# Kernel optimization log

Hardware: AMD Instinct MI355X
Metric: run time of the kernel (lower is better)

The kernel has to match this reference:

```python
import jax, jax.numpy as jnp
import numpy as np

N = 20000      # atom nodes
E_UND = 200000 # undirected edges -> E = 2*E_UND directed, stored as interleaved reverse pairs
D = 128        # hid_dim
H = 4          # heads (fixed in MVMP)
DEPTH = 3


def _build_graph():
    rng = np.random.default_rng(0)
    u_chain = np.arange(N - 1)
    v_chain = u_chain + 1
    n_extra = E_UND - (N - 1)
    ue = rng.integers(0, N, n_extra)
    ve = rng.integers(0, N, n_extra)
    ve = np.where(ue == ve, (ve + 1) % N, ve)
    u = np.concatenate([u_chain, ue])
    v = np.concatenate([v_chain, ve])
    # interleave so that edge 2k = u->v and edge 2k+1 = v->u (reverse_edge pairing)
    src = np.stack([u, v], 1).reshape(-1).astype(np.int32)
    dst = np.stack([v, u], 1).reshape(-1).astype(np.int32)
    return jnp.asarray(src), jnp.asarray(dst)


def setup_inputs() -> dict:
    key = jax.random.key(0)
    ks = jax.random.split(key, 10)
    src, dst = _build_graph()
    E = src.shape[0]
    s = 1.0 / np.sqrt(D)

    def lin(k, shape):
        return (jax.random.normal(k, shape, jnp.float32) * s).astype(jnp.float32)

    return {
        "f": jax.random.normal(ks[0], (N, D), jnp.float32),
        "x": jax.random.normal(ks[1], (E, D), jnp.float32),
        "src": src,
        "dst": dst,
        "Wq": lin(ks[2], (D, D)), "bq": jnp.zeros((D,), jnp.float32),
        "Wk": lin(ks[3], (D, D)), "bk": jnp.zeros((D,), jnp.float32),
        "Wv": lin(ks[4], (D, D)), "bv": jnp.zeros((D,), jnp.float32),
        "Wo": lin(ks[5], (D, D)), "bo": jnp.zeros((D,), jnp.float32),
        "W_mp": lin(ks[6], (DEPTH - 1, D, D)),
        "b_mp": jnp.zeros((DEPTH - 1, D), jnp.float32),
        "W_last": lin(ks[7], (3 * D, D)),
        "b_last": jnp.zeros((D,), jnp.float32),
    }


def _mailbox_attention(f_h, h, dst, Wq, bq, Wk, bk, Wv, bv, Wo, bo):
    """add_attn: per-node MHA with query = node state, keys/values = incoming edge msgs.
    Implemented as an edge-segment softmax (no padding), equivalent to DGL degree bucketing."""
    n = f_h.shape[0]
    dk = D // H
    q = (f_h @ Wq + bq).reshape(n, H, dk)     # [N,H,dk]
    k = (h @ Wk + bk).reshape(-1, H, dk)      # [E,H,dk]
    v = (h @ Wv + bv).reshape(-1, H, dk)      # [E,H,dk]
    scores = jnp.einsum("ehd,ehd->eh", q[dst], k) / jnp.sqrt(jnp.float32(dk))  # [E,H]
    smax = jax.ops.segment_max(scores, dst, num_segments=n)   # [N,H]
    p = jnp.exp(scores - smax[dst])
    denom = jax.ops.segment_sum(p, dst, num_segments=n)       # [N,H]
    ctx = jax.ops.segment_sum(p[:, :, None] * v, dst, num_segments=n) / denom[:, :, None]
    out = ctx.reshape(n, D) @ Wo + bo
    return out + f_h  # residual in add_attn


def reference(f, x, src, dst, Wq, bq, Wk, bk, Wv, bv, Wo, bo, W_mp, b_mp, W_last, b_last):
    n, E = f.shape[0], x.shape[0]
    f_h = f          # init_node: f_h = f.clone()
    h = x            # init_edge: h = x.clone()
    for i in range(DEPTH - 1):
        # multi_update_all: copy_e('h','m') then add_attn on node states
        f_h = _mailbox_attention(f_h, h, dst, Wq, bq, Wk, bk, Wv, bv, Wo, bo)
        # rev_h = reverse_edge(h): swap interleaved pairs
        rev_h = h.reshape(E // 2, 2, D)[:, ::-1, :].reshape(E, D)
        # del_reverse_message: m = f_h[src] - rev_h
        m = f_h[src] - rev_h
        # update_edge: h = relu(x + Linear_i(m))
        h = jax.nn.relu(x + m @ W_mp[i] + b_mp[i])
    # final: copy_e('h','mail') then update_node with Linear(3D->D)
    mail = jax.ops.segment_sum(h, dst, num_segments=n)
    return jnp.concatenate([mail, f_h, f], axis=1) @ W_last + b_last
```

## Files before the change

### kernel.cpp

```cpp
#include <hip/hip_runtime.h>
#include <hip/hip_bf16.h>

typedef __attribute__((ext_vector_type(8))) short bf16x8;
typedef __attribute__((ext_vector_type(4))) float f32x4;

__device__ __forceinline__ unsigned short f2bf(float f) {
    unsigned u = __float_as_uint(f);
    unsigned r = (u + 0x7FFFu + ((u >> 16) & 1u)) >> 16;
    return (unsigned short)r;
}
__device__ __forceinline__ float bf2f(unsigned short b) {
    return __uint_as_float(((unsigned)b) << 16);
}
__device__ __forceinline__ unsigned pack2(float a, float b) {
    return (unsigned)f2bf(a) | ((unsigned)f2bf(b) << 16);
}
__device__ __forceinline__ unsigned pksub(unsigned a, unsigned b) {
    float r0 = bf2f((unsigned short)(a & 0xffff)) - bf2f((unsigned short)(b & 0xffff));
    float r1 = bf2f((unsigned short)(a >> 16))    - bf2f((unsigned short)(b >> 16));
    return pack2(r0, r1);
}
#define EXP2(x) __builtin_amdgcn_exp2f(x)

__device__ __forceinline__ void gload_lds16(const void* g, void* l) {
    __builtin_amdgcn_global_load_lds(
        (const __attribute__((address_space(1))) unsigned int*)g,
        (__attribute__((address_space(3))) unsigned int*)l,
        16, 0, 0);
}

__global__ __launch_bounds__(512, 2) void gemm_q512(
    const unsigned short* __restrict__ A, const unsigned short* __restrict__ WT,
    const float* __restrict__ bias, unsigned short* __restrict__ out, int M)
{
    __shared__ __align__(16) unsigned short As[64 * 128];

    const int t = threadIdx.x, wave = t >> 6, lane = t & 63;
    const int lr = lane & 15, lk = lane >> 4;

    bf16x8 Bf[4][4];
    f32x4 bs[4];
#pragma unroll
    for (int fn = 0; fn < 4; fn++) {
        const int col0 = wave * 64 + fn * 16 + lk * 4;
        bs[fn] = *reinterpret_cast<const f32x4*>(bias + col0);
        const int n = wave * 64 + fn * 16 + lr;
#pragma unroll
        for (int kk = 0; kk < 4; kk++)
            Bf[kk][fn] = *reinterpret_cast<const bf16x8*>(WT + n * 128 + kk * 32 + lk * 8);
    }

    const int row0 = blockIdx.x * 64;
#pragma unroll
    for (int i = 0; i < 2; i++) {
        const int flat = (i * 512 + t) * 16;
        const int r = flat >> 8, c = (flat >> 4) & 15;
        int gr = row0 + r; if (gr >= M) gr = M - 1;
        const void* g = A + (size_t)gr * 128 + ((c ^ (r & 7)) << 3);
        void* l = (void*)((char*)&As[0] + (size_t)(i * 512 + wave * 64) * 16 + 0);
        gload_lds16(g, l);
    }
    __syncthreads();

    f32x4 acc[4][4];
#pragma unroll
    for (int a = 0; a < 4; a++)
#pragma unroll
        for (int b = 0; b < 4; b++) acc[a][b] = (f32x4){0.f, 0.f, 0.f, 0.f};

#pragma unroll
    for (int kk = 0; kk < 4; kk++) {
        bf16x8 af[4];
#pragma unroll
        for (int fm = 0; fm < 4; fm++) {
            const int r = fm * 16 + lr;
            const int c = (kk * 4 + lk) ^ (r & 7);
            af[fm] = *reinterpret_cast<const bf16x8*>(&As[r * 128 + c * 8]);
        }
#pragma unroll
        for (int fm = 0; fm < 4; fm++)
#pragma unroll
            for (int fn = 0; fn < 4; fn++)
                acc[fm][fn] = __builtin_amdgcn_mfma_f32_16x16x32_bf16(
                    Bf[kk][fn], af[fm], acc[fm][fn], 0, 0, 0);
    }

#pragma unroll
    for (int fm = 0; fm < 4; fm++) {
        const int row = row0 + fm * 16 + lr;
        if (row < M) {
#pragma unroll
            for (int fn = 0; fn < 4; fn++) {
                const int col0 = wave * 64 + fn * 16 + lk * 4;
                f32x4 vv = acc[fm][fn] + bs[fn];
                uint2 o; o.x = pack2(vv[0], vv[1]); o.y = pack2(vv[2], vv[3]);
                *reinterpret_cast<uint2*>(out + (size_t)row * 512 + col0) = o;
            }
        }
    }
}

__global__ __launch_bounds__(256, 2) void gemm_k512(
    const unsigned short* __restrict__ A, const unsigned short* __restrict__ WT,
    const float* __restrict__ bias, float* __restrict__ f_h,
    unsigned short* __restrict__ f_hb, int M)
{
    __shared__ __align__(16) unsigned short As[64 * 512];

    const int t = threadIdx.x, wave = t >> 6, lane = t & 63;
    const int lr = lane & 15, lk = lane >> 4;

    bf16x8 Bf[16][2];
    f32x4 bs[2];
#pragma unroll
    for (int fn = 0; fn < 2; fn++) {
        const int col0 = wave * 32 + fn * 16 + lk * 4;
        bs[fn] = *reinterpret_cast<const f32x4*>(bias + col0);
        const int n = wave * 32 + fn * 16 + lr;
#pragma unroll
        for (int kk = 0; kk < 16; kk++)
            Bf[kk][fn] = *reinterpret_cast<const bf16x8*>(WT + n * 512 + kk * 32 + lk * 8);
    }

    const int row0 = blockIdx.x * 64;
#pragma unroll
    for (int i = 0; i < 16; i++) {
        const int flat = (i * 256 + t) * 16;
        const int r = flat >> 10, c = (flat >> 4) & 63;
        int gr = row0 + r; if (gr >= M) gr = M - 1;
        const void* g = A + (size_t)gr * 512 + ((c ^ (r & 7)) << 3);
        void* l = (void*)((char*)&As[0] + (size_t)(i * 256 + wave * 64) * 16);
        gload_lds16(g, l);
    }
    __syncthreads();

    f32x4 acc[4][2];
#pragma unroll
    for (int a = 0; a < 4; a++)
#pragma unroll
        for (int b = 0; b < 2; b++) acc[a][b] = (f32x4){0.f, 0.f, 0.f, 0.f};

#pragma unroll
    for (int kk = 0; kk < 16; kk++) {
        bf16x8 af[4];
#pragma unroll
        for (int fm = 0; fm < 4; fm++) {
            const int r = fm * 16 + lr;
            const int c = (kk * 4 + lk) ^ (r & 7);
            af[fm] = *reinterpret_cast<const bf16x8*>(&As[r * 512 + c * 8]);
        }
#pragma unroll
        for (int fm = 0; fm < 4; fm++)
#pragma unroll
            for (int fn = 0; fn < 2; fn++)
                acc[fm][fn] = __builtin_amdgcn_mfma_f32_16x16x32_bf16(
                    Bf[kk][fn], af[fm], acc[fm][fn], 0, 0, 0);
    }

#pragma unroll
    for (int fm = 0; fm < 4; fm++) {
        const int row = row0 + fm * 16 + lr;
        if (row < M) {
#pragma unroll
            for (int fn = 0; fn < 2; fn++) {
                const int col0 = wave * 32 + fn * 16 + lk * 4;
                const size_t off = (size_t)row * 128 + col0;
                f32x4 vv = acc[fm][fn] + bs[fn];
                vv += *reinterpret_cast<const f32x4*>(f_h + off);
                *reinterpret_cast<f32x4*>(f_h + off) = vv;
                uint2 o; o.x = pack2(vv[0], vv[1]); o.y = pack2(vv[2], vv[3]);
                *reinterpret_cast<uint2*>(f_hb + off) = o;
            }
        }
    }
}

__global__ __launch_bounds__(256, 3) void gemm_mrelu(
    const unsigned short* __restrict__ f_hb, const unsigned short* __restrict__ h,
    const int* __restrict__ src, const unsigned short* __restrict__ WT,
    const float* __restrict__ bias, const unsigned short* __restrict__ resx,
    unsigned short* __restrict__ out, int E, int ntiles)
{
    __shared__ __align__(16) unsigned short As[2][64 * 128];

    const int t = threadIdx.x, wave = t >> 6, lane = t & 63;
    const int lr = lane & 15, lk = lane >> 4;

    bf16x8 Bf[4][2];
    f32x4 bs[2];
#pragma unroll
    for (int fn = 0; fn < 2; fn++) {
        const int col0 = wave * 32 + fn * 16 + lk * 4;
        bs[fn] = *reinterpret_cast<const f32x4*>(bias + col0);
        const int n = wave * 32 + fn * 16 + lr;
#pragma unroll
        for (int kk = 0; kk < 4; kk++)
            Bf[kk][fn] = *reinterpret_cast<const bf16x8*>(WT + n * 128 + kk * 32 + lk * 8);
    }

    uint4 Lh[4], Lf[4];
    auto load_t = [&](int row0) {
#pragma unroll
        for (int i = 0; i < 4; i++) {
            const int flat = (wave * 4 + i) * 1024 + lane * 16;
            const int r = flat >> 8, c = (flat >> 4) & 15;
            int e = row0 + r; if (e >= E) e = E - 1;
            Lh[i] = *reinterpret_cast<const uint4*>(h + (size_t)(e ^ 1) * 128 + c * 8);
            const int se = src[e];
            Lf[i] = *reinterpret_cast<const uint4*>(f_hb + (size_t)se * 128 + c * 8);
        }
    };
    auto write_t = [&](int buf) {
#pragma unroll
        for (int i = 0; i < 4; i++) {
            const int flat = (wave * 4 + i) * 1024 + lane * 16;
            const int r = flat >> 8, c = (flat >> 4) & 15;
            uint4 d;
            d.x = pksub(Lf[i].x, Lh[i].x); d.y = pksub(Lf[i].y, Lh[i].y);
            d.z = pksub(Lf[i].z, Lh[i].z); d.w = pksub(Lf[i].w, Lh[i].w);
            *reinterpret_cast<uint4*>(&As[buf][r * 128 + ((c ^ (r & 7)) << 3)]) = d;
        }
    };

    int tt = blockIdx.x;
    if (tt >= ntiles) return;
    load_t(tt * 64);
    write_t(0);
    int cur = 0;
    __syncthreads();

    for (; tt < ntiles; tt += gridDim.x) {
        const int nxt = tt + gridDim.x;
        if (nxt < ntiles) load_t(nxt * 64);

        f32x4 acc[4][2];
#pragma unroll
        for (int a = 0; a < 4; a++)
#pragma unroll
            for (int b = 0; b < 2; b++) acc[a][b] = (f32x4){0.f, 0.f, 0.f, 0.f};

#pragma unroll
        for (int kk = 0; kk < 4; kk++) {
            bf16x8 af[4];
#pragma unroll
            for (int fm = 0; fm < 4; fm++) {
                const int r = fm * 16 + lr;
                const int c = (kk * 4 + lk) ^ (r & 7);
                af[fm] = *reinterpret_cast<const bf16x8*>(&As[cur][r * 128 + c * 8]);
            }
#pragma unroll
            for (int fm = 0; fm < 4; fm++)
#pragma unroll
                for (int fn = 0; fn < 2; fn++)
                    acc[fm][fn] = __builtin_amdgcn_mfma_f32_16x16x32_bf16(
                        Bf[kk][fn], af[fm], acc[fm][fn], 0, 0, 0);
        }

        const int row0 = tt * 64;
#pragma unroll
        for (int fm = 0; fm < 4; fm++) {
            const int row = row0 + fm * 16 + lr;
            if (row < E) {
#pragma unroll
                for (int fn = 0; fn < 2; fn++) {
                    const int col0 = wave * 32 + fn * 16 + lk * 4;
                    const size_t off = (size_t)row * 128 + col0;
                    f32x4 vv = acc[fm][fn] + bs[fn];
                    uint2 rb = *reinterpret_cast<const uint2*>(resx + off);
                    vv[0] += bf2f((unsigned short)(rb.x & 0xffff));
                    vv[1] += bf2f((unsigned short)(rb.x >> 16));
                    vv[2] += bf2f((unsigned short)(rb.y & 0xffff));
                    vv[3] += bf2f((unsigned short)(rb.y >> 16));
                    vv[0] = fmaxf(vv[0], 0.f); vv[1] = fmaxf(vv[1], 0.f);
                    vv[2] = fmaxf(vv[2], 0.f); vv[3] = fmaxf(vv[3], 0.f);
                    uint2 o; o.x = pack2(vv[0], vv[1]); o.y = pack2(vv[2], vv[3]);
                    *reinterpret_cast<uint2*>(out + off) = o;
                }
            }
        }

        if (nxt < ntiles) write_t(cur ^ 1);
        __syncthreads();
        cur ^= 1;
    }
}

__global__ __launch_bounds__(256, 2) void gemm_final(
    const unsigned short* __restrict__ A0, const unsigned short* __restrict__ A1,
    const unsigned short* __restrict__ A2,
    const unsigned short* __restrict__ W0T, const unsigned short* __restrict__ W1T,
    const unsigned short* __restrict__ W2T,
    const float* __restrict__ bias, float* __restrict__ out, int M)
{
    __shared__ __align__(16) unsigned short As[3][64 * 128];

    const int t = threadIdx.x, wave = t >> 6, lane = t & 63;
    const int lr = lane & 15, lk = lane >> 4;

    const unsigned short* Asrc[3] = { A0, A1, A2 };
    const unsigned short* Wsrc[3] = { W0T, W1T, W2T };

    bf16x8 Bf[12][2];
    f32x4 bs[2];
#pragma unroll
    for (int fn = 0; fn < 2; fn++) {
        const int col0 = wave * 32 + fn * 16 + lk * 4;
        bs[fn] = *reinterpret_cast<const f32x4*>(bias + col0);
        const int n = wave * 32 + fn * 16 + lr;
#pragma unroll
        for (int b = 0; b < 3; b++)
#pragma unroll
            for (int kk = 0; kk < 4; kk++)
                Bf[b * 4 + kk][fn] = *reinterpret_cast<const bf16x8*>(
                    Wsrc[b] + n * 128 + kk * 32 + lk * 8);
    }

    const int row0 = blockIdx.x * 64;
#pragma unroll
    for (int b = 0; b < 3; b++) {
#pragma unroll
        for (int i = 0; i < 4; i++) {
            const int flat = (wave * 4 + i) * 1024 + lane * 16;
            const int r = flat >> 8, c = (flat >> 4) & 15;
            int gr = row0 + r; if (gr >= M) gr = M - 1;
            const void* g = Asrc[b] + (size_t)gr * 128 + ((c ^ (r & 7)) << 3);
            void* l = (void*)((char*)&As[b][0] + (size_t)(wave * 4 + i) * 1024);
            gload_lds16(g, l);
        }
    }
    __syncthreads();

    f32x4 acc[4][2];
#pragma unroll
    for (int a = 0; a < 4; a++)
#pragma unroll
        for (int b = 0; b < 2; b++) acc[a][b] = (f32x4){0.f, 0.f, 0.f, 0.f};

#pragma unroll
    for (int b = 0; b < 3; b++) {
#pragma unroll
        for (int kk = 0; kk < 4; kk++) {
            bf16x8 af[4];
#pragma unroll
            for (int fm = 0; fm < 4; fm++) {
                const int r = fm * 16 + lr;
                const int c = (kk * 4 + lk) ^ (r & 7);
                af[fm] = *reinterpret_cast<const bf16x8*>(&As[b][r * 128 + c * 8]);
            }
#pragma unroll
            for (int fm = 0; fm < 4; fm++)
#pragma unroll
                for (int fn = 0; fn < 2; fn++)
                    acc[fm][fn] = __builtin_amdgcn_mfma_f32_16x16x32_bf16(
                        Bf[b * 4 + kk][fn], af[fm], acc[fm][fn], 0, 0, 0);
        }
    }

#pragma unroll
    for (int fm = 0; fm < 4; fm++) {
        const int row = row0 + fm * 16 + lr;
        if (row < M) {
#pragma unroll
            for (int fn = 0; fn < 2; fn++) {
                const int col0 = wave * 32 + fn * 16 + lk * 4;
                *reinterpret_cast<f32x4*>(out + (size_t)row * 128 + col0) =
                    acc[fm][fn] + bs[fn];
            }
        }
    }
}

__global__ void hist_kernel(const int* __restrict__ dst, int* __restrict__ deg, int E_) {
    int e = blockIdx.x * 256 + threadIdx.x;
    if (e < E_) atomicAdd(&deg[dst[e]], 1);
}

__global__ __launch_bounds__(1024) void scan_kernel(
    const int* __restrict__ deg, int* __restrict__ rowptr,
    int* __restrict__ cursor, int N_)
{
    __shared__ int part[1024];
    const int t = threadIdx.x;
    const int chunk = (N_ + 1023) >> 10;
    const int base = t * chunk;
    int s = 0;
    for (int i = 0; i < chunk; i++) {
        int idx = base + i;
        if (idx < N_) s += deg[idx];
    }
    part[t] = s;
    __syncthreads();
    for (int off = 1; off < 1024; off <<= 1) {
        int v = (t >= off) ? part[t - off] : 0;
        __syncthreads();
        part[t] += v;
        __syncthreads();
    }
    int run = (t == 0) ? 0 : part[t - 1];
    for (int i = 0; i < chunk; i++) {
        int idx = base + i;
        if (idx < N_) {
            rowptr[idx] = run;
            cursor[idx] = run;
            run += deg[idx];
        }
    }
    if (t == 1023) rowptr[N_] = part[1023];
}

__global__ void scatter_kernel(const int* __restrict__ dst, int* __restrict__ cursor,
                               int* __restrict__ eidx, int E_) {
    int e = blockIdx.x * 256 + threadIdx.x;
    if (e >= E_) return;
    int pos = atomicAdd(&cursor[dst[e]], 1);
    eidx[pos] = e;
}

__global__ __launch_bounds__(256) void attn_fused(
    const unsigned short* __restrict__ qkt, const unsigned short* __restrict__ h,
    const int* __restrict__ rowptr, const int* __restrict__ eidx,
    unsigned short* __restrict__ whm, int N_)
{
    const int n = blockIdx.x * 4 + (threadIdx.x >> 6);
    if (n >= N_) return;
    const int lane = threadIdx.x & 63;
    const int g = lane >> 4, s = lane & 15;

    const int beg = rowptr[n], end = rowptr[n + 1];
    unsigned short* outp = whm + (size_t)n * 512 + g * 128 + s * 8;
    if (beg == end) {
        *reinterpret_cast<uint2*>(outp) = make_uint2(0u, 0u);
        *reinterpret_cast<uint2*>(outp + 4) = make_uint2(0u, 0u);
        return;
    }

    float qk[4][8];
#pragma unroll
    for (int hd = 0; hd < 4; hd++) {
        uint4 u = *reinterpret_cast<const uint4*>(qkt + (size_t)n * 512 + hd * 128 + s * 8);
        qk[hd][0] = bf2f((unsigned short)(u.x & 0xffff)); qk[hd][1] = bf2f((unsigned short)(u.x >> 16));
        qk[hd][2] = bf2f((unsigned short)(u.y & 0xffff)); qk[hd][3] = bf2f((unsigned short)(u.y >> 16));
        qk[hd][4] = bf2f((unsigned short)(u.z & 0xffff)); qk[hd][5] = bf2f((unsigned short)(u.z >> 16));
        qk[hd][6] = bf2f((unsigned short)(u.w & 0xffff)); qk[hd][7] = bf2f((unsigned short)(u.w >> 16));
    }

    float m[4], l[4], a[4][8];
#pragma unroll
    for (int hd = 0; hd < 4; hd++) {
        m[hd] = -3.0e38f; l[hd] = 0.f;
#pragma unroll
        for (int j = 0; j < 8; j++) a[hd][j] = 0.f;
    }

    const int T = (end - beg + 3) >> 2;
    int idx = beg + g;
    uint4 hv = make_uint4(0u, 0u, 0u, 0u);
    if (idx < end) hv = *reinterpret_cast<const uint4*>(h + (size_t)eidx[idx] * 128 + s * 8);

    for (int it = 0; it < T; it++) {
        const uint4 hc = hv;
        const bool valid = (idx < end);
        const int nidx = idx + 4;
        if (nidx < end) hv = *reinterpret_cast<const uint4*>(h + (size_t)eidx[nidx] * 128 + s * 8);
        idx = nidx;

        float hf[8];
        hf[0] = bf2f((unsigned short)(hc.x & 0xffff)); hf[1] = bf2f((unsigned short)(hc.x >> 16));
        hf[2] = bf2f((unsigned short)(hc.y & 0xffff)); hf[3] = bf2f((unsigned short)(hc.y >> 16));
        hf[4] = bf2f((unsigned short)(hc.z & 0xffff)); hf[5] = bf2f((unsigned short)(hc.z >> 16));
        hf[6] = bf2f((unsigned short)(hc.w & 0xffff)); hf[7] = bf2f((unsigned short)(hc.w >> 16));

        float part[4];
#pragma unroll
        for (int hd = 0; hd < 4; hd++) {
            float pp = 0.f;
#pragma unroll
            for (int j = 0; j < 8; j++) pp += qk[hd][j] * hf[j];
            part[hd] = pp;
        }
#pragma unroll
        for (int off = 1; off < 16; off <<= 1) {
#pragma unroll
            for (int hd = 0; hd < 4; hd++)
                part[hd] += __shfl_xor(part[hd], off, 64);
        }

        if (valid) {
#pragma unroll
            for (int hd = 0; hd < 4; hd++) {
                const float sv = part[hd];
                const float mn = fmaxf(m[hd], sv);
                const float sc = EXP2(m[hd] - mn);
                const float pp = EXP2(sv - mn);
                l[hd] = l[hd] * sc + pp;
#pragma unroll
                for (int j = 0; j < 8; j++) a[hd][j] = a[hd][j] * sc + pp * hf[j];
                m[hd] = mn;
            }
        }
    }

#pragma unroll
    for (int off = 16; off <= 32; off <<= 1) {
#pragma unroll
        for (int hd = 0; hd < 4; hd++) {
            const float mo = __shfl_xor(m[hd], off, 64);
            const float lo = __shfl_xor(l[hd], off, 64);
            const float mn = fmaxf(m[hd], mo);
            const float sc = EXP2(m[hd] - mn);
            const float so = EXP2(mo - mn);
            l[hd] = l[hd] * sc + lo * so;
#pragma unroll
            for (int j = 0; j < 8; j++) {
                const float ao = __shfl_xor(a[hd][j], off, 64);
                a[hd][j] = a[hd][j] * sc + ao * so;
            }
            m[hd] = mn;
        }
    }

#pragma unroll
    for (int hd = 0; hd < 4; hd++) {
        if (g == hd) {
            const float rl = 1.f / l[hd];
            uint4 o;
            o.x = pack2(a[hd][0] * rl, a[hd][1] * rl);
            o.y = pack2(a[hd][2] * rl, a[hd][3] * rl);
            o.z = pack2(a[hd][4] * rl, a[hd][5] * rl);
            o.w = pack2(a[hd][6] * rl, a[hd][7] * rl);
            *reinterpret_cast<uint4*>(outp) = o;
        }
    }
}

__global__ __launch_bounds__(256) void mail_csr(
    const unsigned short* __restrict__ h,
    const int* __restrict__ rowptr, const int* __restrict__ eidx,
    unsigned short* __restrict__ mailb, int N_)
{
    const int n = blockIdx.x * 4 + (threadIdx.x >> 6);
    if (n >= N_) return;
    const int lane = threadIdx.x & 63;
    const int g = lane >> 4, s = lane & 15;

    const int beg = rowptr[n], end = rowptr[n + 1];

    float a[8];
#pragma unroll
    for (int j = 0; j < 8; j++) a[j] = 0.f;

    const int T = (end - beg + 3) >> 2;
    int idx = beg + g;
    uint4 hv = make_uint4(0u, 0u, 0u, 0u);
    if (idx < end) hv = *reinterpret_cast<const uint4*>(h + (size_t)eidx[idx] * 128 + s * 8);

    for (int it = 0; it < T; it++) {
        const uint4 hc = hv;
        const bool valid = (idx < end);
        const int nidx = idx + 4;
        if (nidx < end) hv = *reinterpret_cast<const uint4*>(h + (size_t)eidx[nidx] * 128 + s * 8);
        idx = nidx;
        if (valid) {
            a[0] += bf2f((unsigned short)(hc.x & 0xffff)); a[1] += bf2f((unsigned short)(hc.x >> 16));
            a[2] += bf2f((unsigned short)(hc.y & 0xffff)); a[3] += bf2f((unsigned short)(hc.y >> 16));
            a[4] += bf2f((unsigned short)(hc.z & 0xffff)); a[5] += bf2f((unsigned short)(hc.z >> 16));
            a[6] += bf2f((unsigned short)(hc.w & 0xffff)); a[7] += bf2f((unsigned short)(hc.w >> 16));
        }
    }
#pragma unroll
    for (int off = 16; off <= 32; off <<= 1)
#pragma unroll
        for (int j = 0; j < 8; j++) a[j] += __shfl_xor(a[j], off, 64);

    if (g == 0) {
        uint4 o;
        o.x = pack2(a[0], a[1]); o.y = pack2(a[2], a[3]);
        o.z = pack2(a[4], a[5]); o.w = pack2(a[6], a[7]);
        *reinterpret_cast<uint4*>(mailb + (size_t)n * 128 + s * 8) = o;
    }
}

struct W5 { const float* p[5]; };

__global__ void cvt_wT(W5 w, unsigned short* __restrict__ out) {
    const float* src = w.p[blockIdx.x];
    unsigned short* dst = out + (size_t)blockIdx.x * 16384;
    for (int idx = threadIdx.x; idx < 16384; idx += 256) {
        const int k = idx >> 7, n = idx & 127;
        dst[n * 128 + k] = f2bf(src[idx]);
    }
}

#define SCORE_SCALE 0.25508994161f

__global__ void mcat_kernel(const float* __restrict__ Wq, const float* __restrict__ Wk,
                            const float* __restrict__ bq,
                            unsigned short* __restrict__ McatT, float* __restrict__ cbias) {
    const int oc = blockIdx.x;
    const int hd = oc >> 7, ip = oc & 127;
    const int a = threadIdx.x;
    const float* wk = Wk + ip * 128 + hd * 32;
    const float* wq = Wq + a * 128 + hd * 32;
    float s = 0.f;
    for (int jj = 0; jj < 32; jj++) s += wq[jj] * wk[jj];
    McatT[(size_t)oc * 128 + a] = f2bf(s * SCORE_SCALE);
    if (a == 0) {
        float c = 0.f;
        for (int jj = 0; jj < 32; jj++) c += bq[hd * 32 + jj] * wk[jj];
        cbias[oc] = c * SCORE_SCALE;
    }
}

__global__ void pcat_kernel(const float* __restrict__ Wv, const float* __restrict__ Wo,
                            unsigned short* __restrict__ PcatT) {
    const int j = blockIdx.x;
    const int k = threadIdx.x;
    const int hd = k >> 7, i = k & 127;
    float s = 0.f;
    for (int cc = 0; cc < 32; cc++)
        s += Wv[i * 128 + hd * 32 + cc] * Wo[(hd * 32 + cc) * 128 + j];
    PcatT[(size_t)j * 512 + k] = f2bf(s);
}

__global__ void bias2_kernel(const float* __restrict__ bv, const float* __restrict__ Wo,
                             const float* __restrict__ bo, float* __restrict__ bias2) {
    const int j = threadIdx.x;
    if (j >= 128) return;
    float s = 0.f;
    for (int c = 0; c < 128; c++) s += bv[c] * Wo[c * 128 + j];
    bias2[j] = s + bo[j];
}

__global__ void cvt_bf16(const float* __restrict__ in, unsigned short* __restrict__ out, long n4) {
    long i = (long)blockIdx.x * 256 + threadIdx.x;
    if (i >= n4) return;
    float4 v = reinterpret_cast<const float4*>(in)[i];
    ushort4 o;
    o.x = f2bf(v.x); o.y = f2bf(v.y); o.z = f2bf(v.z); o.w = f2bf(v.w);
    reinterpret_cast<ushort4*>(out)[i] = o;
}

__global__ void prep_f(const float* __restrict__ f, unsigned short* __restrict__ fb,
                       float* __restrict__ f_h, int n4) {
    int i = blockIdx.x * 256 + threadIdx.x;
    if (i >= n4) return;
    float4 v = reinterpret_cast<const float4*>(f)[i];
    reinterpret_cast<float4*>(f_h)[i] = v;
    ushort4 o;
    o.x = f2bf(v.x); o.y = f2bf(v.y); o.z = f2bf(v.z); o.w = f2bf(v.w);
    reinterpret_cast<ushort4*>(fb)[i] = o;
}

extern "C" void kernel_launch(void* const* d_in, const int* in_sizes, int n_in,
                              void* d_out, int out_size, void* d_ws, size_t ws_size,
                              hipStream_t stream)
{
    const float* f      = (const float*)d_in[0];
    const float* x      = (const float*)d_in[1];
    const int*   src    = (const int*)d_in[2];
    const int*   dst    = (const int*)d_in[3];
    const float* Wq     = (const float*)d_in[4];
    const float* bq     = (const float*)d_in[5];
    const float* Wk     = (const float*)d_in[6];
    const float* bk     = (const float*)d_in[7];
    const float* Wv     = (const float*)d_in[8];
    const float* bv     = (const float*)d_in[9];
    const float* Wo     = (const float*)d_in[10];
    const float* bo     = (const float*)d_in[11];
    const float* W_mp   = (const float*)d_in[12];
    const float* b_mp   = (const float*)d_in[13];
    const float* W_last = (const float*)d_in[14];
    const float* b_last = (const float*)d_in[15];
    (void)bk;

    const int N = in_sizes[0] / 128;
    const int E = in_sizes[1] / 128;

    char* p = (char*)d_ws;
    auto take = [&](size_t bytes) { char* r = p; p += (bytes + 255) & ~(size_t)255; return r; };
    unsigned short* w5T   = (unsigned short*)take(5 * 16384 * 2);
    unsigned short* McatT = (unsigned short*)take(512 * 128 * 2);
    unsigned short* PcatT = (unsigned short*)take(128 * 512 * 2);
    float* cbias  = (float*)take(512 * 4);
    float* bias2  = (float*)take(128 * 4);
    unsigned short* xb    = (unsigned short*)take((size_t)E * 128 * 2);
    unsigned short* h1    = (unsigned short*)take((size_t)E * 128 * 2);
    unsigned short* h2    = (unsigned short*)take((size_t)E * 128 * 2);
    unsigned short* fb    = (unsigned short*)take((size_t)N * 128 * 2);
    unsigned short* f_hb  = (unsigned short*)take((size_t)N * 128 * 2);
    unsigned short* qkt   = (unsigned short*)take((size_t)N * 512 * 2);
    unsigned short* whm   = (unsigned short*)take((size_t)N * 512 * 2);
    unsigned short* mailb = (unsigned short*)take((size_t)N * 128 * 2);
    float* f_h    = (float*)take((size_t)N * 128 * 4);
    int* deg      = (int*)take((size_t)N * 4);
    int* rowptr   = (int*)take((size_t)(N + 1) * 4);
    int* cursor   = (int*)take((size_t)N * 4);
    int* eidx     = (int*)take((size_t)E * 4);

    const unsigned short* Wm0T = w5T + 0 * 16384;
    const unsigned short* Wm1T = w5T + 1 * 16384;
    const unsigned short* WL0T = w5T + 2 * 16384;
    const unsigned short* WL1T = w5T + 3 * 16384;
    const unsigned short* WL2T = w5T + 4 * 16384;

    W5 w5;
    w5.p[0] = W_mp; w5.p[1] = W_mp + 16384;
    w5.p[2] = W_last; w5.p[3] = W_last + 16384; w5.p[4] = W_last + 32768;

    cvt_wT<<<5, 256, 0, stream>>>(w5, w5T);
    mcat_kernel<<<512, 128, 0, stream>>>(Wq, Wk, bq, McatT, cbias);
    pcat_kernel<<<128, 512, 0, stream>>>(Wv, Wo, PcatT);
    bias2_kernel<<<1, 128, 0, stream>>>(bv, Wo, bo, bias2);
    cvt_bf16<<<(int)(((long)E * 32 + 255) / 256), 256, 0, stream>>>(x, xb, (long)E * 32);
    prep_f<<<(N * 32 + 255) / 256, 256, 0, stream>>>(f, fb, f_h, N * 32);

    hipMemsetAsync(deg, 0, (size_t)N * 4, stream);
    hist_kernel<<<(E + 255) / 256, 256, 0, stream>>>(dst, deg, E);
    scan_kernel<<<1, 1024, 0, stream>>>(deg, rowptr, cursor, N);
    scatter_kernel<<<(E + 255) / 256, 256, 0, stream>>>(dst, cursor, eidx, E);

    const int ntN = (N + 63) / 64;
    const int ntE = (E + 63) / 64;
    const int gNode = (N + 3) / 4;
    const int gMrelu = (ntE < 1280) ? ntE : 1280;

    const unsigned short* hc = xb;
    unsigned short* houts[2] = { h1, h2 };
    for (int it = 0; it < 2; it++) {
        const unsigned short* fh_in = (it == 0) ? fb : f_hb;
        gemm_q512<<<ntN, 512, 0, stream>>>(fh_in, McatT, cbias, qkt, N);
        attn_fused<<<gNode, 256, 0, stream>>>(qkt, hc, rowptr, eidx, whm, N);
        gemm_k512<<<ntN, 256, 0, stream>>>(whm, PcatT, bias2, f_h, f_hb, N);
        gemm_mrelu<<<gMrelu, 256, 0, stream>>>(
            f_hb, hc, src, (it == 0) ? Wm0T : Wm1T, b_mp + (size_t)it * 128,
            xb, houts[it], E, ntE);
        hc = houts[it];
    }

    mail_csr<<<gNode, 256, 0, stream>>>(hc, rowptr, eidx, mailb, N);

    gemm_final<<<ntN, 256, 0, stream>>>(
        mailb, f_hb, fb, WL0T, WL1T, WL2T, b_last, (float*)d_out, N);
}
```

Before: 554.9 us.

## Split edge GEMM by linearity: precompute f_h@W per node, gather result

Uses linearity, (f_h[src]-rev_h)@W = (f_h@W)[src] - rev_h@W. A new small node GEMM computes f_h@W once per node, and the edge GEMM then streams h straight into LDS with async global-to-LDS loads. The reverse-pair swap is handled by reading row lr^1 from LDS, and the per-node product is gathered in the epilogue. The attention cross-lane reduction is also restructured into a butterfly that exchanges fewer values, and the edge-kernel grid size changes. The cost is an extra kernel launch plus an extra rounding of the node product to bf16.

```diff
diff --git a/kernel.cpp b/kernel.cpp
--- a/kernel.cpp
+++ b/kernel.cpp
@@ -14,11 +14,6 @@
 }
 __device__ __forceinline__ unsigned pack2(float a, float b) {
     return (unsigned)f2bf(a) | ((unsigned)f2bf(b) << 16);
-}
-__device__ __forceinline__ unsigned pksub(unsigned a, unsigned b) {
-    float r0 = bf2f((unsigned short)(a & 0xffff)) - bf2f((unsigned short)(b & 0xffff));
-    float r1 = bf2f((unsigned short)(a >> 16))    - bf2f((unsigned short)(b >> 16));
-    return pack2(r0, r1);
 }
 #define EXP2(x) __builtin_amdgcn_exp2f(x)
 
@@ -27,6 +22,16 @@
         (const __attribute__((address_space(1))) unsigned int*)g,
         (__attribute__((address_space(3))) unsigned int*)l,
         16, 0, 0);
+}
+
+__device__ __forceinline__ void mergeSt(float& Km, float& Kl, float (&Ka)[8],
+                                        float rm, float rl, const float (&ra)[8]) {
+    const float mn = fmaxf(Km, rm);
+    const float c1 = EXP2(Km - mn), c2 = EXP2(rm - mn);
+    Kl = Kl * c1 + rl * c2;
+#pragma unroll
+    for (int j = 0; j < 8; j++) Ka[j] = Ka[j] * c1 + ra[j] * c2;
+    Km = mn;
 }
 
 __global__ __launch_bounds__(512, 2) void gemm_q512(
@@ -175,9 +180,78 @@
     }
 }
 
-__global__ __launch_bounds__(256, 3) void gemm_mrelu(
-    const unsigned short* __restrict__ f_hb, const unsigned short* __restrict__ h,
-    const int* __restrict__ src, const unsigned short* __restrict__ WT,
+__global__ __launch_bounds__(256, 2) void gemm_n128(
+    const unsigned short* __restrict__ A, const unsigned short* __restrict__ WT,
+    unsigned short* __restrict__ out, int M)
+{
+    __shared__ __align__(16) unsigned short As[64 * 128];
+
+    const int t = threadIdx.x, wave = t >> 6, lane = t & 63;
+    const int lr = lane & 15, lk = lane >> 4;
+
+    bf16x8 Bf[4][2];
+#pragma unroll
+    for (int fn = 0; fn < 2; fn++) {
+        const int n = wave * 32 + fn * 16 + lr;
+#pragma unroll
+        for (int kk = 0; kk < 4; kk++)
+            Bf[kk][fn] = *reinterpret_cast<const bf16x8*>(WT + n * 128 + kk * 32 + lk * 8);
+    }
+
+    const int row0 = blockIdx.x * 64;
+#pragma unroll
+    for (int i = 0; i < 4; i++) {
+        const int flat = (wave * 4 + i) * 1024 + lane * 16;
+        const int r = flat >> 8, c = (flat >> 4) & 15;
+        int gr = row0 + r; if (gr >= M) gr = M - 1;
+        const void* g = A + (size_t)gr * 128 + ((c ^ (r & 7)) << 3);
+        void* l = (void*)((char*)&As[0] + (size_t)(wave * 4 + i) * 1024);
+        gload_lds16(g, l);
+    }
+    __syncthreads();
+
+    f32x4 acc[4][2];
+#pragma unroll
+    for (int a = 0; a < 4; a++)
+#pragma unroll
+        for (int b = 0; b < 2; b++) acc[a][b] = (f32x4){0.f, 0.f, 0.f, 0.f};
+
+#pragma unroll
+    for (int kk = 0; kk < 4; kk++) {
+        bf16x8 af[4];
+#pragma unroll
+        for (int fm = 0; fm < 4; fm++) {
+            const int r = fm * 16 + lr;
+            const int c = (kk * 4 + lk) ^ (r & 7);
+            af[fm] = *reinterpret_cast<const bf16x8*>(&As[r * 128 + c * 8]);
+        }
+#pragma unroll
+        for (int fm = 0; fm < 4; fm++)
+#pragma unroll
+            for (int fn = 0; fn < 2; fn++)
+                acc[fm][fn] = __builtin_amdgcn_mfma_f32_16x16x32_bf16(
+                    Bf[kk][fn], af[fm], acc[fm][fn], 0, 0, 0);
+    }
+
+#pragma unroll
+    for (int fm = 0; fm < 4; fm++) {
+        const int row = row0 + fm * 16 + lr;
+        if (row < M) {
+#pragma unroll
+            for (int fn = 0; fn < 2; fn++) {
+                const int col0 = wave * 32 + fn * 16 + lk * 4;
+                uint2 o;
+                o.x = pack2(acc[fm][fn][0], acc[fm][fn][1]);
+                o.y = pack2(acc[fm][fn][2], acc[fm][fn][3]);
+                *reinterpret_cast<uint2*>(out + (size_t)row * 128 + col0) = o;
+            }
+        }
+    }
+}
+
+__global__ __launch_bounds__(256, 3) void gemm_hw(
+    const unsigned short* __restrict__ h, const int* __restrict__ src,
+    const unsigned short* __restrict__ gnb, const unsigned short* __restrict__ WT,
     const float* __restrict__ bias, const unsigned short* __restrict__ resx,
     unsigned short* __restrict__ out, int E, int ntiles)
 {
@@ -198,40 +272,40 @@
             Bf[kk][fn] = *reinterpret_cast<const bf16x8*>(WT + n * 128 + kk * 32 + lk * 8);
     }
 
-    uint4 Lh[4], Lf[4];
-    auto load_t = [&](int row0) {
+    auto stage = [&](int buf, int row0) {
 #pragma unroll
         for (int i = 0; i < 4; i++) {
             const int flat = (wave * 4 + i) * 1024 + lane * 16;
             const int r = flat >> 8, c = (flat >> 4) & 15;
-            int e = row0 + r; if (e >= E) e = E - 1;
-            Lh[i] = *reinterpret_cast<const uint4*>(h + (size_t)(e ^ 1) * 128 + c * 8);
-            const int se = src[e];
-            Lf[i] = *reinterpret_cast<const uint4*>(f_hb + (size_t)se * 128 + c * 8);
-        }
-    };
-    auto write_t = [&](int buf) {
-#pragma unroll
-        for (int i = 0; i < 4; i++) {
-            const int flat = (wave * 4 + i) * 1024 + lane * 16;
-            const int r = flat >> 8, c = (flat >> 4) & 15;
-            uint4 d;
-            d.x = pksub(Lf[i].x, Lh[i].x); d.y = pksub(Lf[i].y, Lh[i].y);
-            d.z = pksub(Lf[i].z, Lh[i].z); d.w = pksub(Lf[i].w, Lh[i].w);
-            *reinterpret_cast<uint4*>(&As[buf][r * 128 + ((c ^ (r & 7)) << 3)]) = d;
+            int gr = row0 + r; if (gr >= E) gr = E - 1;
+            const void* g = h + (size_t)gr * 128 + ((c ^ (r & 7)) << 3);
+            void* l = (void*)((char*)&As[buf][0] + (size_t)(wave * 4 + i) * 1024);
+            gload_lds16(g, l);
         }
     };
 
     int tt = blockIdx.x;
     if (tt >= ntiles) return;
-    load_t(tt * 64);
-    write_t(0);
+    stage(0, tt * 64);
+    __syncthreads();
     int cur = 0;
-    __syncthreads();
 
     for (; tt < ntiles; tt += gridDim.x) {
         const int nxt = tt + gridDim.x;
-        if (nxt < ntiles) load_t(nxt * 64);
+        if (nxt < ntiles) stage(cur ^ 1, nxt * 64);
+
+        const int row0 = tt * 64;
+
+        uint2 gnv[4][2];
+#pragma unroll
+        for (int fm = 0; fm < 4; fm++) {
+            int row = row0 + fm * 16 + lr; if (row >= E) row = E - 1;
+            const int sr = src[row];
+#pragma unroll
+            for (int fn = 0; fn < 2; fn++)
+                gnv[fm][fn] = *reinterpret_cast<const uint2*>(
+                    gnb + (size_t)sr * 128 + wave * 32 + fn * 16 + lk * 4);
+        }
 
         f32x4 acc[4][2];
 #pragma unroll
@@ -244,9 +318,9 @@
             bf16x8 af[4];
 #pragma unroll
             for (int fm = 0; fm < 4; fm++) {
-                const int r = fm * 16 + lr;
-                const int c = (kk * 4 + lk) ^ (r & 7);
-                af[fm] = *reinterpret_cast<const bf16x8*>(&As[cur][r * 128 + c * 8]);
+                const int rr = fm * 16 + (lr ^ 1);
+                const int cc = (kk * 4 + lk) ^ (rr & 7);
+                af[fm] = *reinterpret_cast<const bf16x8*>(&As[cur][rr * 128 + cc * 8]);
             }
 #pragma unroll
             for (int fm = 0; fm < 4; fm++)
@@ -256,7 +330,6 @@
                         Bf[kk][fn], af[fm], acc[fm][fn], 0, 0, 0);
         }
 
-        const int row0 = tt * 64;
 #pragma unroll
         for (int fm = 0; fm < 4; fm++) {
             const int row = row0 + fm * 16 + lr;
@@ -265,8 +338,13 @@
                 for (int fn = 0; fn < 2; fn++) {
                     const int col0 = wave * 32 + fn * 16 + lk * 4;
                     const size_t off = (size_t)row * 128 + col0;
-                    f32x4 vv = acc[fm][fn] + bs[fn];
-                    uint2 rb = *reinterpret_cast<const uint2*>(resx + off);
+                    f32x4 vv = bs[fn] - acc[fm][fn];
+                    const uint2 gb = gnv[fm][fn];
+                    vv[0] += bf2f((unsigned short)(gb.x & 0xffff));
+                    vv[1] += bf2f((unsigned short)(gb.x >> 16));
+                    vv[2] += bf2f((unsigned short)(gb.y & 0xffff));
+                    vv[3] += bf2f((unsigned short)(gb.y >> 16));
+                    const uint2 rb = *reinterpret_cast<const uint2*>(resx + off);
                     vv[0] += bf2f((unsigned short)(rb.x & 0xffff));
                     vv[1] += bf2f((unsigned short)(rb.x >> 16));
                     vv[2] += bf2f((unsigned short)(rb.y & 0xffff));
@@ -279,7 +357,6 @@
             }
         }
 
-        if (nxt < ntiles) write_t(cur ^ 1);
         __syncthreads();
         cur ^= 1;
     }
@@ -500,37 +577,53 @@
         }
     }
 
-#pragma unroll
-    for (int off = 16; off <= 32; off <<= 1) {
-#pragma unroll
-        for (int hd = 0; hd < 4; hd++) {
-            const float mo = __shfl_xor(m[hd], off, 64);
-            const float lo = __shfl_xor(l[hd], off, 64);
-            const float mn = fmaxf(m[hd], mo);
-            const float sc = EXP2(m[hd] - mn);
-            const float so = EXP2(mo - mn);
-            l[hd] = l[hd] * sc + lo * so;
-#pragma unroll
-            for (int j = 0; j < 8; j++) {
-                const float ao = __shfl_xor(a[hd][j], off, 64);
-                a[hd][j] = a[hd][j] * sc + ao * so;
-            }
-            m[hd] = mn;
-        }
-    }
-
-#pragma unroll
-    for (int hd = 0; hd < 4; hd++) {
-        if (g == hd) {
-            const float rl = 1.f / l[hd];
-            uint4 o;
-            o.x = pack2(a[hd][0] * rl, a[hd][1] * rl);
-            o.y = pack2(a[hd][2] * rl, a[hd][3] * rl);
-            o.z = pack2(a[hd][4] * rl, a[hd][5] * rl);
-            o.w = pack2(a[hd][6] * rl, a[hd][7] * rl);
-            *reinterpret_cast<uint4*>(outp) = o;
-        }
-    }
+    const bool lo = (g < 2);
+    const bool evn = ((g & 1) == 0);
+    float kAm = lo ? m[0] : m[2], kAl = lo ? l[0] : l[2];
+    float kBm = lo ? m[1] : m[3], kBl = lo ? l[1] : l[3];
+    float sAm = lo ? m[2] : m[0], sAl = lo ? l[2] : l[0];
+    float sBm = lo ? m[3] : m[1], sBl = lo ? l[3] : l[1];
+    float kAa[8], kBa[8], sAa[8], sBa[8];
+#pragma unroll
+    for (int j = 0; j < 8; j++) {
+        kAa[j] = lo ? a[0][j] : a[2][j];
+        kBa[j] = lo ? a[1][j] : a[3][j];
+        sAa[j] = lo ? a[2][j] : a[0][j];
+        sBa[j] = lo ? a[3][j] : a[1][j];
+    }
+    {
+        float rm = __shfl_xor(sAm, 32, 64), rl = __shfl_xor(sAl, 32, 64);
+        float ra[8];
+#pragma unroll
+        for (int j = 0; j < 8; j++) ra[j] = __shfl_xor(sAa[j], 32, 64);
+        mergeSt(kAm, kAl, kAa, rm, rl, ra);
+        rm = __shfl_xor(sBm, 32, 64); rl = __shfl_xor(sBl, 32, 64);
+#pragma unroll
+        for (int j = 0; j < 8; j++) ra[j] = __shfl_xor(sBa[j], 32, 64);
+        mergeSt(kBm, kBl, kBa, rm, rl, ra);
+    }
+    float Km = evn ? kAm : kBm, Kl = evn ? kAl : kBl;
+    float Sm = evn ? kBm : kAm, Sl = evn ? kBl : kAl;
+    float Ka[8], Sa[8];
+#pragma unroll
+    for (int j = 0; j < 8; j++) {
+        Ka[j] = evn ? kAa[j] : kBa[j];
+        Sa[j] = evn ? kBa[j] : kAa[j];
+    }
+    {
+        float rm = __shfl_xor(Sm, 16, 64), rl = __shfl_xor(Sl, 16, 64);
+        float ra[8];
+#pragma unroll
+        for (int j = 0; j < 8; j++) ra[j] = __shfl_xor(Sa[j], 16, 64);
+        mergeSt(Km, Kl, Ka, rm, rl, ra);
+    }
+    const float rl_ = 1.f / Kl;
+    uint4 o;
+    o.x = pack2(Ka[0] * rl_, Ka[1] * rl_);
+    o.y = pack2(Ka[2] * rl_, Ka[3] * rl_);
+    o.z = pack2(Ka[4] * rl_, Ka[5] * rl_);
+    o.w = pack2(Ka[6] * rl_, Ka[7] * rl_);
+    *reinterpret_cast<uint4*>(outp) = o;
 }
 
 __global__ __launch_bounds__(256) void mail_csr(
@@ -688,6 +781,7 @@
     unsigned short* h2    = (unsigned short*)take((size_t)E * 128 * 2);
     unsigned short* fb    = (unsigned short*)take((size_t)N * 128 * 2);
     unsigned short* f_hb  = (unsigned short*)take((size_t)N * 128 * 2);
+    unsigned short* gnb   = (unsigned short*)take((size_t)N * 128 * 2);
     unsigned short* qkt   = (unsigned short*)take((size_t)N * 512 * 2);
     unsigned short* whm   = (unsigned short*)take((size_t)N * 512 * 2);
     unsigned short* mailb = (unsigned short*)take((size_t)N * 128 * 2);
@@ -722,18 +816,19 @@
     const int ntN = (N + 63) / 64;
     const int ntE = (E + 63) / 64;
     const int gNode = (N + 3) / 4;
-    const int gMrelu = (ntE < 1280) ? ntE : 1280;
+    const int gHw = (ntE < 1024) ? ntE : 1024;
 
     const unsigned short* hc = xb;
     unsigned short* houts[2] = { h1, h2 };
     for (int it = 0; it < 2; it++) {
         const unsigned short* fh_in = (it == 0) ? fb : f_hb;
+        const unsigned short* WmT = (it == 0) ? Wm0T : Wm1T;
         gemm_q512<<<ntN, 512, 0, stream>>>(fh_in, McatT, cbias, qkt, N);
         attn_fused<<<gNode, 256, 0, stream>>>(qkt, hc, rowptr, eidx, whm, N);
         gemm_k512<<<ntN, 256, 0, stream>>>(whm, PcatT, bias2, f_h, f_hb, N);
-        gemm_mrelu<<<gMrelu, 256, 0, stream>>>(
-            f_hb, hc, src, (it == 0) ? Wm0T : Wm1T, b_mp + (size_t)it * 128,
-            xb, houts[it], E, ntE);
+        gemm_n128<<<ntN, 256, 0, stream>>>(f_hb, WmT, gnb, N);
+        gemm_hw<<<gHw, 256, 0, stream>>>(
+            hc, src, gnb, WmT, b_mp + (size_t)it * 128, xb, houts[it], E, ntE);
         hc = houts[it];
     }
 
```

After: 598.0 us. +7.8%, slower.
